# Kernel optimization log

Measured on AMD Instinct MI355X. Metric: run time of the kernel, lower is better.

Reference implementation:

```python
import jax, jax.numpy as jnp
import numpy as np

N, E = 50000, 150000
IN, HID, LAT, EF, HE = 16, 32, 16, 8, 128


def _p(k, shape, fan_in):
    return jax.random.normal(k, shape, jnp.float32) / np.float32(np.sqrt(fan_in))


def setup_inputs() -> dict:
    key = jax.random.key(0)
    ks = jax.random.split(key, 32)
    inp = {
        "x": jax.random.normal(ks[0], (N, IN), jnp.float32),
        "edge_index": jax.random.randint(ks[1], (2, E), 0, N, dtype=jnp.int64),
        "edge_attr": jax.random.uniform(ks[2], (E, EF), jnp.float32),
    }
    # per-conv params: edge-MLP (w1,b1,w2,b2), root weight, bias
    dims = {"c1": (IN, HID), "c2": (HID, HID), "cmu": (HID, LAT), "clv": (HID, LAT)}
    i = 3
    for name, (din, dout) in dims.items():
        inp[f"{name}_w1"] = _p(ks[i], (EF, HE), EF)
        inp[f"{name}_b1"] = jnp.zeros((HE,), jnp.float32)
        inp[f"{name}_w2"] = _p(ks[i + 1], (HE, din * dout), HE)
        inp[f"{name}_b2"] = jnp.zeros((din * dout,), jnp.float32)
        inp[f"{name}_root"] = _p(ks[i + 2], (din, dout), din)
        inp[f"{name}_bias"] = jnp.zeros((dout,), jnp.float32)
        i += 3
    return inp


def _nnconv(x, src, dst, ea, w1, b1, w2, b2, root, bias, din, dout, mean):
    # edge MLP -> per-edge weight matrix [E, din, dout]
    h = jax.nn.relu(ea @ w1 + b1)
    W = (h @ w2 + b2).reshape(-1, din, dout)
    # gather source features, per-edge matmul, scatter-reduce to targets
    msg = jnp.einsum('ei,eio->eo', x[src], W)  # [E, dout]
    agg = jax.ops.segment_sum(msg, dst, num_segments=x.shape[0])
    if mean:
        cnt = jax.ops.segment_sum(jnp.ones((dst.shape[0],), x.dtype), dst,
                                  num_segments=x.shape[0])
        agg = agg / jnp.maximum(cnt, 1.0)[:, None]
    return agg + x @ root + bias


def reference(x, edge_index, edge_attr,
              c1_w1, c1_b1, c1_w2, c1_b2, c1_root, c1_bias,
              c2_w1, c2_b1, c2_w2, c2_b2, c2_root, c2_bias,
              cmu_w1, cmu_b1, cmu_w2, cmu_b2, cmu_root, cmu_bias,
              clv_w1, clv_b1, clv_w2, clv_b2, clv_root, clv_bias):
    src, dst = edge_index[0], edge_index[1]
    h = jax.nn.relu(_nnconv(x, src, dst, edge_attr, c1_w1, c1_b1, c1_w2, c1_b2,
                            c1_root, c1_bias, IN, HID, True))
    h = jax.nn.relu(_nnconv(h, src, dst, edge_attr, c2_w1, c2_b1, c2_w2, c2_b2,
                            c2_root, c2_bias, HID, HID, True))
    mu = _nnconv(h, src, dst, edge_attr, cmu_w1, cmu_b1, cmu_w2, cmu_b2,
                 cmu_root, cmu_bias, HID, LAT, False)
    logvar = _nnconv(h, src, dst, edge_attr, clv_w1, clv_b1, clv_w2, clv_b2,
                     clv_root, clv_bias, HID, LAT, False)
    return mu, logvar
```

## Files before the change

kernel.cpp:

```cpp
#include <hip/hip_runtime.h>

typedef __attribute__((ext_vector_type(8))) _Float16 half8;
typedef __attribute__((ext_vector_type(4))) _Float16 half4v;
typedef __attribute__((ext_vector_type(2))) _Float16 half2v;
typedef __attribute__((ext_vector_type(4))) float f32x4;

constexpr int NN  = 50000;
constexpr int NE  = 150000;
constexpr int IN  = 16;
constexpr int HID = 32;
constexpr int LAT = 16;
constexpr int EF  = 8;
constexpr int HE  = 128;
constexpr int NTILE = NE / 16;
constexpr int HSTR  = HE + 2;

constexpr int SCB = 256;
constexpr int NSB = (NN + SCB - 1) / SCB;

union XU {
  half2v h2[4];
  half8  h8;
  _Float16 h[8];
};

__global__ void count_kernel(const int* __restrict__ dst, int* __restrict__ cnt) {
  int e = blockIdx.x * blockDim.x + threadIdx.x;
  if (e < NE) atomicAdd(&cnt[dst[e]], 1);
}

__launch_bounds__(SCB)
__global__ void scan1(const int* __restrict__ cnt, int* __restrict__ bsum) {
  __shared__ int sdata[SCB];
  const int i = blockIdx.x * SCB + threadIdx.x;
  sdata[threadIdx.x] = (i < NN) ? cnt[i] : 0;
  __syncthreads();
  for (int off = SCB / 2; off > 0; off >>= 1) {
    if (threadIdx.x < off) sdata[threadIdx.x] += sdata[threadIdx.x + off];
    __syncthreads();
  }
  if (threadIdx.x == 0) bsum[blockIdx.x] = sdata[0];
}

__launch_bounds__(SCB)
__global__ void scan2(int* __restrict__ bsum) {
  __shared__ int sdata[SCB];
  const int t = threadIdx.x;
  const int v = (t < NSB) ? bsum[t] : 0;
  sdata[t] = v;
  __syncthreads();
  for (int off = 1; off < SCB; off <<= 1) {
    int u = (t >= off) ? sdata[t - off] : 0;
    __syncthreads();
    sdata[t] += u;
    __syncthreads();
  }
  if (t < NSB) bsum[t] = sdata[t] - v;
}

__launch_bounds__(SCB)
__global__ void scan3(const int* __restrict__ cnt, const int* __restrict__ bsum,
                      int* __restrict__ rowptr, int* __restrict__ wptr) {
  __shared__ int sdata[SCB];
  const int i = blockIdx.x * SCB + threadIdx.x;
  const int t = threadIdx.x;
  const int v = (i < NN) ? cnt[i] : 0;
  sdata[t] = v;
  __syncthreads();
  for (int off = 1; off < SCB; off <<= 1) {
    int u = (t >= off) ? sdata[t - off] : 0;
    __syncthreads();
    sdata[t] += u;
    __syncthreads();
  }
  const int excl = sdata[t] - v + bsum[blockIdx.x];
  if (i < NN) {
    rowptr[i] = excl;
    wptr[i]   = excl;
  }
  if (i == NN - 1) rowptr[NN] = NE;
}

__global__ void fill_kernel(const int* __restrict__ dst, int* __restrict__ wptr,
                            int* __restrict__ epos) {
  int e = blockIdx.x * blockDim.x + threadIdx.x;
  if (e < NE) epos[e] = atomicAdd(&wptr[dst[e]], 1);
}

__global__ void swizzle_kernel(const float* __restrict__ w2, const float* __restrict__ b2,
                               const float* __restrict__ w1,
                               _Float16* __restrict__ w2h, float* __restrict__ w1t,
                               int DIN_, int DOUT_) {
  int idx = blockIdx.x * blockDim.x + threadIdx.x;
  if (idx < HE * EF) {
    int kk = idx / EF, i = idx % EF;
    w1t[idx] = w1[i * HE + kk];
  }
  int tot = HSTR * DIN_ * DOUT_;
  if (idx >= tot) return;
  int i  = idx % DIN_;
  int o  = (idx / DIN_) % DOUT_;
  int kk = idx / (DIN_ * DOUT_);
  float v = 0.0f;
  if (kk < HE)       v = w2[(size_t)kk * DIN_ * DOUT_ + i * DOUT_ + o];
  else if (kk == HE) v = b2[i * DOUT_ + o];
  w2h[idx] = (_Float16)v;
}

template <int DIN, int DOUT, bool DUAL>
__launch_bounds__(128)
__global__ void nnconv_mfma(const float* __restrict__ xin,
                            const int*   __restrict__ src,
                            const float* __restrict__ ea,
                            const float* __restrict__ w1tA,
                            const float* __restrict__ b1A,
                            const float* __restrict__ w1tB,
                            const float* __restrict__ b1B,
                            const _Float16* __restrict__ w2hA,
                            const _Float16* __restrict__ w2hB,
                            const int*   __restrict__ epos,
                            _Float16* __restrict__ msgA,
                            _Float16* __restrict__ msgB)
{
  constexpr int KKSTEP  = 32 / DIN;
  constexpr int CHS     = 8 / KKSTEP;
  constexpr int BSTRIDE = KKSTEP * DOUT * DIN;
  constexpr int TILES   = 4;
  constexpr int NTAB    = DUAL ? 2 : 1;

  __shared__ _Float16 h_s[2 * NTAB * 128 * 8];

  const int tid  = threadIdx.x;
  const int wave = tid >> 6;
  const int lane = tid & 63;
  const int eb   = blockIdx.x * 128;

  float eav[EF];
  {
    const int e = eb + tid;
    float4 v0 = make_float4(0.f, 0.f, 0.f, 0.f), v1 = v0;
    if (e < NE) {
      const float4* p = (const float4*)(ea + (size_t)e * EF);
      v0 = p[0]; v1 = p[1];
    }
    eav[0] = v0.x; eav[1] = v0.y; eav[2] = v0.z; eav[3] = v0.w;
    eav[4] = v1.x; eav[5] = v1.y; eav[6] = v1.z; eav[7] = v1.w;
  }

  auto build_chunk = [&](const float* __restrict__ w1t,
                         const float* __restrict__ b1,
                         int c, _Float16* __restrict__ dst) {
    const int kk0 = c * 8;
    const float4 bq0 = *(const float4*)&b1[kk0];
    const float4 bq1 = *(const float4*)&b1[kk0 + 4];
    const float bk[8] = {bq0.x, bq0.y, bq0.z, bq0.w, bq1.x, bq1.y, bq1.z, bq1.w};
    XU hr;
#pragma unroll
    for (int j = 0; j < 8; j++) {
      const int kk = kk0 + j;
      const float4 wa = *(const float4*)&w1t[kk * EF];
      const float4 wb = *(const float4*)&w1t[kk * EF + 4];
      float hv = bk[j];
      hv = fmaf(eav[0], wa.x, hv); hv = fmaf(eav[1], wa.y, hv);
      hv = fmaf(eav[2], wa.z, hv); hv = fmaf(eav[3], wa.w, hv);
      hv = fmaf(eav[4], wb.x, hv); hv = fmaf(eav[5], wb.y, hv);
      hv = fmaf(eav[6], wb.z, hv); hv = fmaf(eav[7], wb.w, hv);
      hv = fmaxf(hv, 0.0f);
      hr.h[j] = (_Float16)hv;
    }
    *(half8*)&dst[tid * 8] = hr.h8;
  };

  const int m = lane & 15, q = lane >> 4;
  const int i0 = (q * 8) % DIN;
  const int kq = (q * 8) / DIN;
  const int tg0 = blockIdx.x * 8 + wave * TILES;

  XU xv[TILES];
#pragma unroll
  for (int t = 0; t < TILES; t++) {
    const int tg = tg0 + t;
    if (tg < NTILE) {
      const int s = src[tg * 16 + m];
      const float4* xp = (const float4*)(xin + (size_t)s * DIN + i0);
      const float4 a = xp[0], b = xp[1];
      xv[t].h2[0] = (half2v){(_Float16)a.x, (_Float16)a.y};
      xv[t].h2[1] = (half2v){(_Float16)a.z, (_Float16)a.w};
      xv[t].h2[2] = (half2v){(_Float16)b.x, (_Float16)b.y};
      xv[t].h2[3] = (half2v){(_Float16)b.z, (_Float16)b.w};
    } else {
#pragma unroll
      for (int j = 0; j < 4; j++) xv[t].h2[j] = (half2v){(_Float16)0.f, (_Float16)0.f};
    }
  }

  f32x4 acc[TILES][2];
#pragma unroll
  for (int t = 0; t < TILES; t++)
#pragma unroll
    for (int f = 0; f < 2; f++) acc[t][f] = (f32x4){0.f, 0.f, 0.f, 0.f};

  int hrow[TILES];
#pragma unroll
  for (int t = 0; t < TILES; t++) hrow[t] = wave * 64 + t * 16 + m;

  auto make_af = [&](const XU& xvt, _Float16 hv) -> XU {
    const half2v hb = (half2v){hv, hv};
    XU af;
#pragma unroll
    for (int j = 0; j < 4; j++) af.h2[j] = xvt.h2[j] * hb;
    return af;
  };

  const _Float16* bp0;
  const _Float16* bp1;
  if (DUAL) {
    bp0 = w2hA + (size_t)(kq * DOUT + m) * DIN + i0;
    bp1 = w2hB + (size_t)(kq * DOUT + m) * DIN + i0;
  } else {
    bp0 = w2hA + (size_t)(kq * DOUT + 0 + m) * DIN + i0;
    bp1 = w2hA + (size_t)(kq * DOUT + 16 + m) * DIN + i0;
  }

#pragma unroll 1
  for (int c = 0; c < 16; c++) {
    _Float16* buf = &h_s[(size_t)(c & 1) * NTAB * 128 * 8];
    build_chunk(w1tA, b1A, c, buf);
    if (DUAL) build_chunk(w1tB, b1B, c, buf + 128 * 8);
    __syncthreads();

    XU hc0[TILES], hc1[TILES];
#pragma unroll
    for (int t = 0; t < TILES; t++)
      hc0[t].h8 = *(const half8*)&buf[hrow[t] * 8];
    if (DUAL) {
#pragma unroll
      for (int t = 0; t < TILES; t++)
        hc1[t].h8 = *(const half8*)&buf[128 * 8 + hrow[t] * 8];
    }

#pragma unroll
    for (int s = 0; s < CHS; s++) {
      const half8 bf0 = *(const half8*)(bp0 + (size_t)(c * CHS + s) * BSTRIDE);
      const half8 bf1 = *(const half8*)(bp1 + (size_t)(c * CHS + s) * BSTRIDE);
#pragma unroll
      for (int t = 0; t < TILES; t++) {
        _Float16 hv0;
        if (DIN == 32) hv0 = hc0[t].h[s];
        else {
          const _Float16 h0 = hc0[t].h[2 * s], h1 = hc0[t].h[2 * s + 1];
          hv0 = kq ? h1 : h0;
        }
        const XU af0 = make_af(xv[t], hv0);
        acc[t][0] = __builtin_amdgcn_mfma_f32_16x16x32_f16(af0.h8, bf0,
                                                           acc[t][0], 0, 0, 0);
        if (DUAL) {
          _Float16 hv1;
          if (DIN == 32) hv1 = hc1[t].h[s];
          else {
            const _Float16 h0 = hc1[t].h[2 * s], h1 = hc1[t].h[2 * s + 1];
            hv1 = kq ? h1 : h0;
          }
          const XU af1 = make_af(xv[t], hv1);
          acc[t][1] = __builtin_amdgcn_mfma_f32_16x16x32_f16(af1.h8, bf1,
                                                             acc[t][1], 0, 0, 0);
        } else {
          acc[t][1] = __builtin_amdgcn_mfma_f32_16x16x32_f16(af0.h8, bf1,
                                                             acc[t][1], 0, 0, 0);
        }
      }
    }
  }

  {
    const half8 bf0 = *(const half8*)(bp0 + (size_t)(128 / KKSTEP) * BSTRIDE);
    const half8 bf1 = *(const half8*)(bp1 + (size_t)(128 / KKSTEP) * BSTRIDE);
#pragma unroll
    for (int t = 0; t < TILES; t++) {
      XU af;
      if (DIN == 32) af = xv[t];
      else {
#pragma unroll
        for (int j = 0; j < 4; j++)
          af.h2[j] = kq ? (half2v){(_Float16)0.f, (_Float16)0.f} : xv[t].h2[j];
      }
      acc[t][0] = __builtin_amdgcn_mfma_f32_16x16x32_f16(af.h8, bf0,
                                                         acc[t][0], 0, 0, 0);
      acc[t][1] = __builtin_amdgcn_mfma_f32_16x16x32_f16(af.h8, bf1,
                                                         acc[t][1], 0, 0, 0);
    }
  }

#pragma unroll
  for (int t = 0; t < TILES; t++) {
    const int tg = tg0 + t;
    if (tg < NTILE) {
      const int ebase = tg * 16 + q * 4;
      const int4 ep = *(const int4*)(epos + ebase);
      const int pr[4] = {ep.x, ep.y, ep.z, ep.w};
      if (DUAL) {
#pragma unroll
        for (int r = 0; r < 4; r++) {
          msgA[(size_t)pr[r] * DOUT + m] = (_Float16)acc[t][0][r];
          msgB[(size_t)pr[r] * DOUT + m] = (_Float16)acc[t][1][r];
        }
      } else {
#pragma unroll
        for (int f = 0; f < 2; f++)
#pragma unroll
          for (int r = 0; r < 4; r++)
            msgA[(size_t)pr[r] * DOUT + f * 16 + m] = (_Float16)acc[t][f][r];
      }
    }
  }
}

template <int DIN, int DOUT, bool MEAN, bool RELU>
__launch_bounds__(256)
__global__ void finish_kernel(const _Float16* __restrict__ msg,
                              const int* __restrict__ rowptr,
                              const float* __restrict__ xin,
                              const float* __restrict__ root,
                              const float* __restrict__ bias,
                              float* __restrict__ out) {
  constexpr int TPN = DOUT / 4;
  const int gid = blockIdx.x * 256 + threadIdx.x;
  const int n = gid / TPN, sub = gid % TPN;
  if (n >= NN) return;
  const int o0 = sub * 4;

  const int r0 = rowptr[n], r1 = rowptr[n + 1];
  float ax = 0.f, ay = 0.f, az = 0.f, aw = 0.f;
  for (int idx = r0; idx < r1; idx++) {
    const half4v mv = *(const half4v*)(msg + (size_t)idx * DOUT + o0);
    ax += (float)mv.x; ay += (float)mv.y; az += (float)mv.z; aw += (float)mv.w;
  }
  const float inv = MEAN ? 1.0f / fmaxf((float)(r1 - r0), 1.0f) : 1.0f;
  float vx = ax * inv + bias[o0 + 0];
  float vy = ay * inv + bias[o0 + 1];
  float vz = az * inv + bias[o0 + 2];
  float vw = aw * inv + bias[o0 + 3];
#pragma unroll
  for (int i = 0; i < DIN; i++) {
    const float xi = xin[(size_t)n * DIN + i];
    const float4 rv = *(const float4*)(root + (size_t)i * DOUT + o0);
    vx = fmaf(xi, rv.x, vx); vy = fmaf(xi, rv.y, vy);
    vz = fmaf(xi, rv.z, vz); vw = fmaf(xi, rv.w, vw);
  }
  if (RELU) {
    vx = fmaxf(vx, 0.f); vy = fmaxf(vy, 0.f);
    vz = fmaxf(vz, 0.f); vw = fmaxf(vw, 0.f);
  }
  *(float4*)(out + (size_t)n * DOUT + o0) = make_float4(vx, vy, vz, vw);
}

template <int DIN>
__launch_bounds__(256)
__global__ void finish_dual(const _Float16* __restrict__ msgA,
                            const _Float16* __restrict__ msgB,
                            const int* __restrict__ rowptr,
                            const float* __restrict__ xin,
                            const float* __restrict__ rootA,
                            const float* __restrict__ biasA,
                            const float* __restrict__ rootB,
                            const float* __restrict__ biasB,
                            float* __restrict__ outA,
                            float* __restrict__ outB) {
  constexpr int TPN = LAT / 4;
  const int gid = blockIdx.x * 256 + threadIdx.x;
  const int n = gid / TPN, sub = gid % TPN;
  if (n >= NN) return;
  const int o0 = sub * 4;

  const int r0 = rowptr[n], r1 = rowptr[n + 1];
  float a0 = 0.f, a1 = 0.f, a2 = 0.f, a3 = 0.f;
  float b0 = 0.f, b1 = 0.f, b2 = 0.f, b3 = 0.f;
  for (int idx = r0; idx < r1; idx++) {
    const half4v ma = *(const half4v*)(msgA + (size_t)idx * LAT + o0);
    const half4v mb = *(const half4v*)(msgB + (size_t)idx * LAT + o0);
    a0 += (float)ma.x; a1 += (float)ma.y; a2 += (float)ma.z; a3 += (float)ma.w;
    b0 += (float)mb.x; b1 += (float)mb.y; b2 += (float)mb.z; b3 += (float)mb.w;
  }
  float va0 = a0 + biasA[o0 + 0], va1 = a1 + biasA[o0 + 1];
  float va2 = a2 + biasA[o0 + 2], va3 = a3 + biasA[o0 + 3];
  float vb0 = b0 + biasB[o0 + 0], vb1 = b1 + biasB[o0 + 1];
  float vb2 = b2 + biasB[o0 + 2], vb3 = b3 + biasB[o0 + 3];
#pragma unroll
  for (int i = 0; i < DIN; i++) {
    const float xi = xin[(size_t)n * DIN + i];
    const float4 ra = *(const float4*)(rootA + (size_t)i * LAT + o0);
    const float4 rb = *(const float4*)(rootB + (size_t)i * LAT + o0);
    va0 = fmaf(xi, ra.x, va0); va1 = fmaf(xi, ra.y, va1);
    va2 = fmaf(xi, ra.z, va2); va3 = fmaf(xi, ra.w, va3);
    vb0 = fmaf(xi, rb.x, vb0); vb1 = fmaf(xi, rb.y, vb1);
    vb2 = fmaf(xi, rb.z, vb2); vb3 = fmaf(xi, rb.w, vb3);
  }
  *(float4*)(outA + (size_t)n * LAT + o0) = make_float4(va0, va1, va2, va3);
  *(float4*)(outB + (size_t)n * LAT + o0) = make_float4(vb0, vb1, vb2, vb3);
}

extern "C" void kernel_launch(void* const* d_in, const int* in_sizes, int n_in,
                              void* d_out, int out_size, void* d_ws, size_t ws_size,
                              hipStream_t stream) {
  const float* x  = (const float*)d_in[0];
  const int*   ei = (const int*)d_in[1];
  const float* ea = (const float*)d_in[2];
  const int* src = ei;
  const int* dst = ei + NE;

  auto P = [&](int c, int j) -> const float* {
    return (const float*)d_in[3 + c * 6 + j];
  };

  float* h1  = (float*)d_ws;
  float* h2  = h1 + (size_t)NN * HID;
  _Float16* msg = (_Float16*)(h2 + (size_t)NN * HID);
  int* cnt    = (int*)(msg + (size_t)NE * 32);
  int* rowptr = cnt + NN;
  int* wptr   = rowptr + 50004;
  int* epos   = wptr + 50004;
  int* bsum   = epos + NE;
  _Float16* w2h_c1 = (_Float16*)(bsum + 256);
  _Float16* w2h_c2 = w2h_c1 + (size_t)HSTR * 32 * 16;
  _Float16* w2h_mu = w2h_c2 + (size_t)HSTR * 32 * 32;
  _Float16* w2h_lv = w2h_mu + (size_t)HSTR * 16 * 32;
  float* w1t_c1 = (float*)(w2h_lv + (size_t)HSTR * 16 * 32);
  float* w1t_c2 = w1t_c1 + HE * EF;
  float* w1t_mu = w1t_c2 + HE * EF;
  float* w1t_lv = w1t_mu + HE * EF;

  _Float16* msgA = msg;
  _Float16* msgB = msg + (size_t)NE * 16;

  float* out_mu = (float*)d_out;
  float* out_lv = out_mu + (size_t)NN * LAT;

  hipMemsetAsync(cnt, 0, (size_t)NN * sizeof(int), stream);
  count_kernel<<<dim3((NE + 255) / 256), dim3(256), 0, stream>>>(dst, cnt);
  scan1<<<dim3(NSB), dim3(SCB), 0, stream>>>(cnt, bsum);
  scan2<<<dim3(1), dim3(SCB), 0, stream>>>(bsum);
  scan3<<<dim3(NSB), dim3(SCB), 0, stream>>>(cnt, bsum, rowptr, wptr);
  fill_kernel<<<dim3((NE + 255) / 256), dim3(256), 0, stream>>>(dst, wptr, epos);

  {
    int t1 = HSTR * 16 * 32, t2 = HSTR * 32 * 32, t3 = HSTR * 32 * 16;
    swizzle_kernel<<<dim3((t1 + 255) / 256), dim3(256), 0, stream>>>(
        P(0, 2), P(0, 3), P(0, 0), w2h_c1, w1t_c1, IN, HID);
    swizzle_kernel<<<dim3((t2 + 255) / 256), dim3(256), 0, stream>>>(
        P(1, 2), P(1, 3), P(1, 0), w2h_c2, w1t_c2, HID, HID);
    swizzle_kernel<<<dim3((t3 + 255) / 256), dim3(256), 0, stream>>>(
        P(2, 2), P(2, 3), P(2, 0), w2h_mu, w1t_mu, HID, LAT);
    swizzle_kernel<<<dim3((t3 + 255) / 256), dim3(256), 0, stream>>>(
        P(3, 2), P(3, 3), P(3, 0), w2h_lv, w1t_lv, HID, LAT);
  }

  const dim3 egrid((NTILE + 7) / 8), eblk(128);

  nnconv_mfma<IN, HID, false><<<egrid, eblk, 0, stream>>>(
      x, src, ea, w1t_c1, P(0, 1), nullptr, nullptr, w2h_c1, nullptr,
      epos, msg, nullptr);
  finish_kernel<IN, HID, true, true>
      <<<dim3((NN * (HID / 4) + 255) / 256), dim3(256), 0, stream>>>(
          msg, rowptr, x, P(0, 4), P(0, 5), h1);

  nnconv_mfma<HID, HID, false><<<egrid, eblk, 0, stream>>>(
      h1, src, ea, w1t_c2, P(1, 1), nullptr, nullptr, w2h_c2, nullptr,
      epos, msg, nullptr);
  finish_kernel<HID, HID, true, true>
      <<<dim3((NN * (HID / 4) + 255) / 256), dim3(256), 0, stream>>>(
          msg, rowptr, h1, P(1, 4), P(1, 5), h2);

  nnconv_mfma<HID, LAT, true><<<egrid, eblk, 0, stream>>>(
      h2, src, ea, w1t_mu, P(2, 1), w1t_lv, P(3, 1), w2h_mu, w2h_lv,
      epos, msgA, msgB);
  finish_dual<HID>
      <<<dim3((NN * (LAT / 4) + 255) / 256), dim3(256), 0, stream>>>(
          msgA, msgB, rowptr, h2, P(2, 4), P(2, 5), P(3, 4), P(3, 5),
          out_mu, out_lv);
}
```

Baseline: 343.6 us.

## Use 256-thread blocks with 2 tiles per wave and split edge-MLP builds

Each 128-edge block now runs 4 waves instead of 2, and each wave handles 2 MFMA tiles instead of 4. The two thread halves build different hidden chunks in parallel: in the dual kernel one half builds the mu table and the other the logvar table, and in the single kernel they build two consecutive chunks, which halves the number of barriers. This spreads the per-edge MLP and the MFMA work over more waves for better latency hiding and occupancy. In exchange, every wave reloads the same B fragments, adding global/L2 traffic per tile.

```diff
diff --git a/kernel.cpp b/kernel.cpp
--- a/kernel.cpp
+++ b/kernel.cpp
@@ -108,7 +108,7 @@
 }
 
 template <int DIN, int DOUT, bool DUAL>
-__launch_bounds__(128)
+__launch_bounds__(256)
 __global__ void nnconv_mfma(const float* __restrict__ xin,
                             const int*   __restrict__ src,
                             const float* __restrict__ ea,
@@ -125,19 +125,19 @@
   constexpr int KKSTEP  = 32 / DIN;
   constexpr int CHS     = 8 / KKSTEP;
   constexpr int BSTRIDE = KKSTEP * DOUT * DIN;
-  constexpr int TILES   = 4;
-  constexpr int NTAB    = DUAL ? 2 : 1;
-
-  __shared__ _Float16 h_s[2 * NTAB * 128 * 8];
+  constexpr int TILES   = 2;
+
+  __shared__ _Float16 h_s[4 * 128 * 8];
 
   const int tid  = threadIdx.x;
   const int wave = tid >> 6;
   const int lane = tid & 63;
+  const int erow = tid & 127;
   const int eb   = blockIdx.x * 128;
 
   float eav[EF];
   {
-    const int e = eb + tid;
+    const int e = eb + erow;
     float4 v0 = make_float4(0.f, 0.f, 0.f, 0.f), v1 = v0;
     if (e < NE) {
       const float4* p = (const float4*)(ea + (size_t)e * EF);
@@ -168,7 +168,7 @@
       hv = fmaxf(hv, 0.0f);
       hr.h[j] = (_Float16)hv;
     }
-    *(half8*)&dst[tid * 8] = hr.h8;
+    *(half8*)&dst[erow * 8] = hr.h8;
   };
 
   const int m = lane & 15, q = lane >> 4;
@@ -202,7 +202,7 @@
 
   int hrow[TILES];
 #pragma unroll
-  for (int t = 0; t < TILES; t++) hrow[t] = wave * 64 + t * 16 + m;
+  for (int t = 0; t < TILES; t++) hrow[t] = wave * 32 + t * 16 + m;
 
   auto make_af = [&](const XU& xvt, _Float16 hv) -> XU {
     const half2v hb = (half2v){hv, hv};
@@ -222,51 +222,76 @@
     bp1 = w2hA + (size_t)(kq * DOUT + 16 + m) * DIN + i0;
   }
 
+  if constexpr (DUAL) {
 #pragma unroll 1
-  for (int c = 0; c < 16; c++) {
-    _Float16* buf = &h_s[(size_t)(c & 1) * NTAB * 128 * 8];
-    build_chunk(w1tA, b1A, c, buf);
-    if (DUAL) build_chunk(w1tB, b1B, c, buf + 128 * 8);
-    __syncthreads();
-
-    XU hc0[TILES], hc1[TILES];
-#pragma unroll
-    for (int t = 0; t < TILES; t++)
-      hc0[t].h8 = *(const half8*)&buf[hrow[t] * 8];
-    if (DUAL) {
-#pragma unroll
-      for (int t = 0; t < TILES; t++)
-        hc1[t].h8 = *(const half8*)&buf[128 * 8 + hrow[t] * 8];
-    }
-
-#pragma unroll
-    for (int s = 0; s < CHS; s++) {
-      const half8 bf0 = *(const half8*)(bp0 + (size_t)(c * CHS + s) * BSTRIDE);
-      const half8 bf1 = *(const half8*)(bp1 + (size_t)(c * CHS + s) * BSTRIDE);
+    for (int c = 0; c < 16; c++) {
+      _Float16* buf = &h_s[(size_t)(c & 1) * 2048];
+      if (tid < 128) build_chunk(w1tA, b1A, c, buf);
+      else           build_chunk(w1tB, b1B, c, buf + 1024);
+      __syncthreads();
+
+      XU hc0[TILES], hc1[TILES];
 #pragma unroll
       for (int t = 0; t < TILES; t++) {
-        _Float16 hv0;
-        if (DIN == 32) hv0 = hc0[t].h[s];
-        else {
-          const _Float16 h0 = hc0[t].h[2 * s], h1 = hc0[t].h[2 * s + 1];
-          hv0 = kq ? h1 : h0;
-        }
-        const XU af0 = make_af(xv[t], hv0);
-        acc[t][0] = __builtin_amdgcn_mfma_f32_16x16x32_f16(af0.h8, bf0,
-                                                           acc[t][0], 0, 0, 0);
-        if (DUAL) {
-          _Float16 hv1;
-          if (DIN == 32) hv1 = hc1[t].h[s];
+        hc0[t].h8 = *(const half8*)&buf[hrow[t] * 8];
+        hc1[t].h8 = *(const half8*)&buf[1024 + hrow[t] * 8];
+      }
+
+#pragma unroll
+      for (int s = 0; s < CHS; s++) {
+        const half8 bf0 = *(const half8*)(bp0 + (size_t)(c * CHS + s) * BSTRIDE);
+        const half8 bf1 = *(const half8*)(bp1 + (size_t)(c * CHS + s) * BSTRIDE);
+#pragma unroll
+        for (int t = 0; t < TILES; t++) {
+          _Float16 hv0, hv1;
+          if (DIN == 32) { hv0 = hc0[t].h[s]; hv1 = hc1[t].h[s]; }
           else {
-            const _Float16 h0 = hc1[t].h[2 * s], h1 = hc1[t].h[2 * s + 1];
-            hv1 = kq ? h1 : h0;
+            hv0 = kq ? hc0[t].h[2 * s + 1] : hc0[t].h[2 * s];
+            hv1 = kq ? hc1[t].h[2 * s + 1] : hc1[t].h[2 * s];
           }
+          const XU af0 = make_af(xv[t], hv0);
+          acc[t][0] = __builtin_amdgcn_mfma_f32_16x16x32_f16(af0.h8, bf0,
+                                                             acc[t][0], 0, 0, 0);
           const XU af1 = make_af(xv[t], hv1);
           acc[t][1] = __builtin_amdgcn_mfma_f32_16x16x32_f16(af1.h8, bf1,
                                                              acc[t][1], 0, 0, 0);
-        } else {
-          acc[t][1] = __builtin_amdgcn_mfma_f32_16x16x32_f16(af0.h8, bf1,
-                                                             acc[t][1], 0, 0, 0);
+        }
+      }
+    }
+  } else {
+#pragma unroll 1
+    for (int p = 0; p < 8; p++) {
+      _Float16* bufE = &h_s[(size_t)(p & 1) * 2048];
+      if (tid < 128) build_chunk(w1tA, b1A, 2 * p,     bufE);
+      else           build_chunk(w1tA, b1A, 2 * p + 1, bufE + 1024);
+      __syncthreads();
+
+#pragma unroll
+      for (int sub = 0; sub < 2; sub++) {
+        const int cc = 2 * p + sub;
+        const _Float16* sb = bufE + sub * 1024;
+        XU hc[TILES];
+#pragma unroll
+        for (int t = 0; t < TILES; t++)
+          hc[t].h8 = *(const half8*)&sb[hrow[t] * 8];
+#pragma unroll
+        for (int s = 0; s < CHS; s++) {
+          const half8 bf0 = *(const half8*)(bp0 + (size_t)(cc * CHS + s) * BSTRIDE);
+          const half8 bf1 = *(const half8*)(bp1 + (size_t)(cc * CHS + s) * BSTRIDE);
+#pragma unroll
+          for (int t = 0; t < TILES; t++) {
+            _Float16 hv;
+            if (DIN == 32) hv = hc[t].h[s];
+            else {
+              const _Float16 h0 = hc[t].h[2 * s], h1 = hc[t].h[2 * s + 1];
+              hv = kq ? h1 : h0;
+            }
+            const XU af = make_af(xv[t], hv);
+            acc[t][0] = __builtin_amdgcn_mfma_f32_16x16x32_f16(af.h8, bf0,
+                                                               acc[t][0], 0, 0, 0);
+            acc[t][1] = __builtin_amdgcn_mfma_f32_16x16x32_f16(af.h8, bf1,
+                                                               acc[t][1], 0, 0, 0);
+          }
         }
       }
     }
@@ -454,7 +479,7 @@
         P(3, 2), P(3, 3), P(3, 0), w2h_lv, w1t_lv, HID, LAT);
   }
 
-  const dim3 egrid((NTILE + 7) / 8), eblk(128);
+  const dim3 egrid((NTILE + 7) / 8), eblk(256);
 
   nnconv_mfma<IN, HID, false><<<egrid, eblk, 0, stream>>>(
       x, src, ea, w1t_c1, P(0, 1), nullptr, nullptr, w2h_c1, nullptr,
```

Result: slower. 405.6 us (+18.0%).
